# Optimization experiments

Measured on AMD Instinct MI355X. Metric: run time of the kernel, lower is better.

Reference implementation:

```python
import jax, jax.numpy as jnp
import numpy as np

N_NODES = 100000
N_EDGES = 3200000
IN_DIM, HID_DIM, OUT_DIM = 128, 8, 1


def _graph_conv(x, src, dst, W, b, n_nodes):
    """DGL GraphConv, norm='both', weight applied before aggregation
    (valid since in_feats > out_feats for both layers).
    out = D_in^{-1/2} * scatter_sum_dst( (D_out^{-1/2} * x W)[src] ) + b
    """
    ones_e = jnp.ones((src.shape[0],), dtype=x.dtype)
    deg_out = jax.ops.segment_sum(ones_e, src, num_segments=n_nodes)
    deg_in = jax.ops.segment_sum(ones_e, dst, num_segments=n_nodes)
    norm_out = jnp.clip(deg_out, 1.0, None) ** -0.5  # [N]
    norm_in = jnp.clip(deg_in, 1.0, None) ** -0.5    # [N]
    h = (x * norm_out[:, None]) @ W                   # [N, out_dim] small GEMM first
    msg = h[src]                                      # [E, out_dim] gather
    agg = jax.ops.segment_sum(msg, dst, num_segments=n_nodes)  # [N, out_dim] scatter
    return agg * norm_in[:, None] + b


def setup_inputs() -> dict:
    key = jax.random.key(0)
    k0, k1, k2, k3, k4, k5, k6 = jax.random.split(key, 7)
    x = jax.random.normal(k0, (N_NODES, IN_DIM), dtype=jnp.float32)
    src = jax.random.randint(k1, (N_EDGES,), 0, N_NODES, dtype=jnp.int64)
    dst = jax.random.randint(k2, (N_EDGES,), 0, N_NODES, dtype=jnp.int64)
    # Glorot-uniform weights as in DGL GraphConv reset_parameters
    lim1 = float(np.sqrt(6.0 / (IN_DIM + HID_DIM)))
    lim2 = float(np.sqrt(6.0 / (HID_DIM + OUT_DIM)))
    W1 = jax.random.uniform(k3, (IN_DIM, HID_DIM), minval=-lim1, maxval=lim1, dtype=jnp.float32)
    b1 = jnp.zeros((HID_DIM,), dtype=jnp.float32)
    W2 = jax.random.uniform(k4, (HID_DIM, OUT_DIM), minval=-lim2, maxval=lim2, dtype=jnp.float32)
    b2 = jnp.zeros((OUT_DIM,), dtype=jnp.float32)
    return {"x": x, "src": src, "dst": dst, "W1": W1, "b1": b1, "W2": W2, "b2": b2}


def reference(x, src, dst, W1, b1, W2, b2):
    h = _graph_conv(x, src, dst, W1, b1, N_NODES)   # conv1: 128 -> 8
    h = jax.nn.relu(h)
    out = _graph_conv(h, src, dst, W2, b2, N_NODES)  # conv2: 8 -> 1
    return out
```

## Files before the change

kernel.cpp:

```cpp
#include <hip/hip_runtime.h>
#include <hip/hip_bf16.h>
#include <hip/hip_fp16.h>

#define IN_DIM 128
#define HID 8
#define TW 256
#define MAXT 512
#define CCH 256
#define CAP 12288

__global__ __launch_bounds__(1024) void pass1AB_kernel(const int* __restrict__ src, const int* __restrict__ dst,
        int* __restrict__ cntS, int* __restrict__ cntD, int E, int RT, int chunk) {
    __shared__ int cs[MAXT], cd[MAXT];
    int t = threadIdx.x, c = blockIdx.x;
    for (int i = t; i < RT; i += 1024) { cs[i] = 0; cd[i] = 0; }
    __syncthreads();
    int lo = c * chunk, hi = min(lo + chunk, E);
    if (lo < hi) {
        const int4* s4 = reinterpret_cast<const int4*>(src);
        const int4* d4 = reinterpret_cast<const int4*>(dst);
        int q0 = lo >> 2, q1 = hi >> 2;
        for (int q = q0 + t; q < q1; q += 1024) {
            int4 s = s4[q], d = d4[q];
            atomicAdd(&cs[s.x >> 8], 1); atomicAdd(&cs[s.y >> 8], 1);
            atomicAdd(&cs[s.z >> 8], 1); atomicAdd(&cs[s.w >> 8], 1);
            atomicAdd(&cd[d.x >> 8], 1); atomicAdd(&cd[d.y >> 8], 1);
            atomicAdd(&cd[d.z >> 8], 1); atomicAdd(&cd[d.w >> 8], 1);
        }
        for (int i = (q1 << 2) + t; i < hi; i += 1024) {
            atomicAdd(&cs[src[i] >> 8], 1);
            atomicAdd(&cd[dst[i] >> 8], 1);
        }
    }
    __syncthreads();
    for (int i = t; i < RT; i += 1024) {
        cntS[(size_t)c * RT + i] = cs[i];
        cntD[(size_t)c * RT + i] = cd[i];
    }
}

__global__ __launch_bounds__(256) void scan1_kernel(int* __restrict__ cntS, int* __restrict__ cntD,
        int* __restrict__ totS, int* __restrict__ totD, int RT) {
    int r = blockIdx.x;
    int* cnt = blockIdx.y ? cntD : cntS;
    int* tot = blockIdx.y ? totD : totS;
    __shared__ int sh[256];
    int t = threadIdx.x;
    int e = cnt[(size_t)t * RT + r];
    sh[t] = e;
    __syncthreads();
    for (int off = 1; off < 256; off <<= 1) {
        int v = (t >= off) ? sh[t - off] : 0;
        __syncthreads();
        sh[t] += v;
        __syncthreads();
    }
    cnt[(size_t)t * RT + r] = sh[t] - e;
    if (t == 255) tot[r] = sh[255];
}

__global__ __launch_bounds__(256) void scan2_kernel(const int* __restrict__ totS, const int* __restrict__ totD,
        int* __restrict__ baseS, int* __restrict__ baseD, int RT) {
    const int* tot = blockIdx.x ? totD : totS;
    int* base = blockIdx.x ? baseD : baseS;
    __shared__ int sh[256];
    int t = threadIdx.x;
    int K = (RT + 255) / 256;
    int vals[4];
    int s = 0;
    for (int k = 0; k < K; ++k) {
        int i = t * K + k;
        int v = (i < RT) ? tot[i] : 0;
        vals[k] = v; s += v;
    }
    sh[t] = s;
    __syncthreads();
    for (int off = 1; off < 256; off <<= 1) {
        int v = (t >= off) ? sh[t - off] : 0;
        __syncthreads();
        sh[t] += v;
        __syncthreads();
    }
    int exc = sh[t] - s;
    for (int k = 0; k < K; ++k) {
        int i = t * K + k;
        if (i < RT) base[i] = exc;
        exc += vals[k];
    }
    if (t == 255) base[RT] = sh[255];
}

__global__ __launch_bounds__(1024) void scatterAB_kernel(const int* __restrict__ src, const int* __restrict__ dst,
        const int* __restrict__ cntS, const int* __restrict__ cntD,
        const int* __restrict__ baseS, const int* __restrict__ baseD,
        unsigned char* __restrict__ bucket_s, unsigned int* __restrict__ bucketT,
        int E, int RT, int chunk) {
    __shared__ int os[MAXT], od[MAXT];
    int t = threadIdx.x;
    int c = ((blockIdx.x & 7) << 5) | (blockIdx.x >> 3);
    for (int i = t; i < RT; i += 1024) {
        os[i] = baseS[i] + cntS[(size_t)c * RT + i];
        od[i] = baseD[i] + cntD[(size_t)c * RT + i];
    }
    __syncthreads();
    int lo = c * chunk, hi = min(lo + chunk, E);
    if (lo >= hi) return;
    const int4* s4 = reinterpret_cast<const int4*>(src);
    const int4* d4 = reinterpret_cast<const int4*>(dst);
    int q0 = lo >> 2, q1 = hi >> 2;
    for (int q = q0 + t; q < q1; q += 1024) {
        int4 s = s4[q], d = d4[q];
        int p;
        p = atomicAdd(&os[s.x >> 8], 1); bucket_s[p] = (unsigned char)(s.x & 255);
        p = atomicAdd(&os[s.y >> 8], 1); bucket_s[p] = (unsigned char)(s.y & 255);
        p = atomicAdd(&os[s.z >> 8], 1); bucket_s[p] = (unsigned char)(s.z & 255);
        p = atomicAdd(&os[s.w >> 8], 1); bucket_s[p] = (unsigned char)(s.w & 255);
        p = atomicAdd(&od[d.x >> 8], 1); bucketT[p] = ((unsigned)s.x << 8) | (unsigned)(d.x & 255);
        p = atomicAdd(&od[d.y >> 8], 1); bucketT[p] = ((unsigned)s.y << 8) | (unsigned)(d.y & 255);
        p = atomicAdd(&od[d.z >> 8], 1); bucketT[p] = ((unsigned)s.z << 8) | (unsigned)(d.z & 255);
        p = atomicAdd(&od[d.w >> 8], 1); bucketT[p] = ((unsigned)s.w << 8) | (unsigned)(d.w & 255);
    }
    for (int i = (q1 << 2) + t; i < hi; i += 1024) {
        int s = src[i], d = dst[i];
        int p = atomicAdd(&os[s >> 8], 1);
        bucket_s[p] = (unsigned char)(s & 255);
        p = atomicAdd(&od[d >> 8], 1);
        bucketT[p] = ((unsigned)s << 8) | (unsigned)(d & 255);
    }
}

__global__ __launch_bounds__(256) void conv1deg_kernel(
        const unsigned char* __restrict__ bucket_s, const int* __restrict__ baseS,
        const float* __restrict__ x, const float* __restrict__ W1,
        float* __restrict__ deg_out, uint4* __restrict__ h4, int N) {
    __shared__ float wt[HID * 132];
    __shared__ int cnt[TW];
    __shared__ float nrmS[TW];
    int r = blockIdx.x, t = threadIdx.x;
    for (int i = t; i < IN_DIM * HID; i += 256) {
        int k = i >> 3, j = i & 7;
        wt[j * 132 + k] = W1[i];
    }
    cnt[t] = 0;
    __syncthreads();
    int lo = baseS[r], hi = baseS[r + 1];
    int a0 = min((lo + 3) & ~3, hi), a1 = max(hi & ~3, a0);
    for (int i = lo + t; i < a0; i += 256) atomicAdd(&cnt[bucket_s[i]], 1);
    const unsigned* w4 = reinterpret_cast<const unsigned*>(bucket_s);
    for (int q = (a0 >> 2) + t; q < (a1 >> 2); q += 256) {
        unsigned w = w4[q];
        atomicAdd(&cnt[w & 255], 1);
        atomicAdd(&cnt[(w >> 8) & 255], 1);
        atomicAdd(&cnt[(w >> 16) & 255], 1);
        atomicAdd(&cnt[w >> 24], 1);
    }
    for (int i = a1 + t; i < hi; i += 256) atomicAdd(&cnt[bucket_s[i]], 1);
    __syncthreads();
    {
        int node = r * TW + t;
        if (node < N) deg_out[node] = (float)cnt[t];
        nrmS[t] = rsqrtf(fmaxf((float)cnt[t], 1.0f));
    }
    __syncthreads();
    int grp = t >> 3, lane = t & 7;
    #pragma unroll
    for (int sweep = 0; sweep < 8; ++sweep) {
        int nl = sweep * 32 + grp;
        int node = r * TW + nl;
        if (node < N) {
            const float4* xp = reinterpret_cast<const float4*>(x + (size_t)node * IN_DIM);
            float4 xv[4];
            #pragma unroll
            for (int m = 0; m < 4; ++m) xv[m] = xp[lane + m * 8];
            float acc[HID];
            #pragma unroll
            for (int j = 0; j < HID; ++j) acc[j] = 0.f;
            #pragma unroll
            for (int j = 0; j < HID; ++j) {
                #pragma unroll
                for (int m = 0; m < 4; ++m) {
                    float4 wv = *reinterpret_cast<const float4*>(&wt[j * 132 + lane * 4 + m * 32]);
                    acc[j] += xv[m].x * wv.x + xv[m].y * wv.y + xv[m].z * wv.z + xv[m].w * wv.w;
                }
            }
            #pragma unroll
            for (int off = 1; off < 8; off <<= 1) {
                #pragma unroll
                for (int j = 0; j < HID; ++j) acc[j] += __shfl_xor(acc[j], off, 64);
            }
            if (lane == 0) {
                float nrm = nrmS[nl];
                __half2 p0 = __floats2half2_rn(acc[0] * nrm, acc[1] * nrm);
                __half2 p1 = __floats2half2_rn(acc[2] * nrm, acc[3] * nrm);
                __half2 p2 = __floats2half2_rn(acc[4] * nrm, acc[5] * nrm);
                __half2 p3 = __floats2half2_rn(acc[6] * nrm, acc[7] * nrm);
                uint4 o;
                o.x = *reinterpret_cast<unsigned*>(&p0);
                o.y = *reinterpret_cast<unsigned*>(&p1);
                o.z = *reinterpret_cast<unsigned*>(&p2);
                o.w = *reinterpret_cast<unsigned*>(&p3);
                h4[node] = o;
            }
        }
    }
}

__device__ __forceinline__ void accAdd(float* acc, uint4 g) {
    __half2 q0 = *reinterpret_cast<__half2*>(&g.x);
    __half2 q1 = *reinterpret_cast<__half2*>(&g.y);
    __half2 q2 = *reinterpret_cast<__half2*>(&g.z);
    __half2 q3 = *reinterpret_cast<__half2*>(&g.w);
    float2 f0 = __half22float2(q0), f1 = __half22float2(q1);
    float2 f2 = __half22float2(q2), f3 = __half22float2(q3);
    acc[0] += f0.x; acc[1] += f0.y;
    acc[2] += f1.x; acc[3] += f1.y;
    acc[4] += f2.x; acc[5] += f2.y;
    acc[6] += f3.x; acc[7] += f3.y;
}

__global__ __launch_bounds__(512) void sortagg1_kernel(
        const unsigned int* __restrict__ bucketT, const int* __restrict__ baseD,
        unsigned int* __restrict__ bucketG, int* __restrict__ row_ptr,
        const uint4* __restrict__ h4, const float* __restrict__ deg_out,
        const float* __restrict__ b1, const float* __restrict__ W2,
        float* __restrict__ h2, int E, int RT, int N) {
    __shared__ unsigned sorted[CAP];
    __shared__ int cnt[TW], scn[TW], start[TW];
    __shared__ float b1s[HID], w2s[HID];
    int r = blockIdx.x, t = threadIdx.x;
    if (t < TW) cnt[t] = 0;
    if (t < HID) { b1s[t] = b1[t]; w2s[t] = W2[t]; }
    __syncthreads();
    int lo = baseD[r], hi = baseD[r + 1], len = hi - lo;
    for (int i = lo + t; i < hi; i += 512) atomicAdd(&cnt[bucketT[i] & 255u], 1);
    __syncthreads();
    if (t < TW) scn[t] = cnt[t];
    __syncthreads();
    for (int off = 1; off < TW; off <<= 1) {
        int v = 0;
        if (t < TW && t >= off) v = scn[t - off];
        __syncthreads();
        if (t < TW) scn[t] += v;
        __syncthreads();
    }
    if (t < TW) {
        start[t] = scn[t] - cnt[t];
        row_ptr[r * TW + t] = lo + scn[t] - cnt[t];
    }
    if (r == 0 && t == 0) row_ptr[RT * TW] = E;
    __syncthreads();
    bool fits = (len <= CAP);
    if (fits) {
        for (int i = lo + t; i < hi; i += 512) {
            unsigned v = bucketT[i];
            int p = atomicAdd(&start[v & 255u], 1);
            sorted[p] = v >> 8;
        }
        __syncthreads();
        for (int i = t; i < len; i += 512) bucketG[lo + i] = sorted[i];
    } else {
        for (int i = lo + t; i < hi; i += 512) {
            unsigned v = bucketT[i];
            int p = atomicAdd(&start[v & 255u], 1);
            bucketG[lo + p] = v >> 8;
        }
        __syncthreads();
    }
    #pragma unroll
    for (int half = 0; half < 2; ++half) {
        int nl = (t >> 2) + half * 128;
        int sub = t & 3;
        int node = r * TW + nl;
        int end = scn[nl], beg = end - cnt[nl];
        float acc[HID];
        #pragma unroll
        for (int j = 0; j < HID; ++j) acc[j] = 0.f;
        if (fits) {
            for (int e = beg + sub; e < end; e += 4) accAdd(acc, h4[sorted[e]]);
        } else {
            for (int e = beg + sub; e < end; e += 4) accAdd(acc, h4[bucketG[lo + e]]);
        }
        #pragma unroll
        for (int off = 1; off < 4; off <<= 1) {
            #pragma unroll
            for (int j = 0; j < HID; ++j) acc[j] += __shfl_xor(acc[j], off, 64);
        }
        if (sub == 0 && node < N) {
            float din = (float)(end - beg);
            float nin = rsqrtf(fmaxf(din, 1.f));
            float nout = rsqrtf(fmaxf(deg_out[node], 1.f));
            float dot = 0.f;
            #pragma unroll
            for (int j = 0; j < HID; ++j) {
                float y = fmaxf(acc[j] * nin + b1s[j], 0.f);
                dot += y * w2s[j];
            }
            h2[node] = dot * nout;
        }
    }
}

__global__ __launch_bounds__(256) void agg2G4_kernel(const unsigned int* __restrict__ bucketG,
        const int* __restrict__ row_ptr, const float* __restrict__ h2,
        const float* __restrict__ b2, float* __restrict__ out, int N) {
    int tid = blockIdx.x * 256 + threadIdx.x;
    int node = tid >> 2, sub = tid & 3;
    int s0 = row_ptr[node], s1 = row_ptr[node + 1];
    float a = 0.f;
    for (int e = s0 + sub; e < s1; e += 4) a += h2[bucketG[e]];
    a += __shfl_xor(a, 1, 64);
    a += __shfl_xor(a, 2, 64);
    if (sub == 0 && node < N) {
        float nin = rsqrtf(fmaxf((float)(s1 - s0), 1.f));
        out[node] = a * nin + b2[0];
    }
}

extern "C" void kernel_launch(void* const* d_in, const int* in_sizes, int n_in,
                              void* d_out, int out_size, void* d_ws, size_t ws_size,
                              hipStream_t stream) {
    const float* x  = (const float*)d_in[0];
    const int* src  = (const int*)d_in[1];
    const int* dst  = (const int*)d_in[2];
    const float* W1 = (const float*)d_in[3];
    const float* b1 = (const float*)d_in[4];
    const float* W2 = (const float*)d_in[5];
    const float* b2 = (const float*)d_in[6];
    float* out = (float*)d_out;

    const int N  = out_size;
    const int E  = in_sizes[1];
    const int RT = (N + TW - 1) / TW;
    const int chunk = (((E + CCH - 1) / CCH) + 3) & ~3;

    float* ws      = (float*)d_ws;
    float* deg_out = ws;
    float* h2      = deg_out + N;
    int*   cntS    = (int*)(h2 + N);
    int*   cntD    = cntS + (size_t)CCH * RT;
    int*   totS    = cntD + (size_t)CCH * RT;
    int*   baseS   = totS + RT;
    int*   totD    = baseS + RT + 1;
    int*   baseD   = totD + RT;
    int*   row_ptr = baseD + RT + 1;
    unsigned int* bucketT = (unsigned int*)(row_ptr + (size_t)RT * TW + 1);
    unsigned int* bucketG = bucketT + E;
    uint4* h4 = (uint4*)(((uintptr_t)(bucketG + E) + 15) & ~(uintptr_t)15);
    unsigned char* bucket_s = (unsigned char*)(h4 + N);

    pass1AB_kernel<<<CCH, 1024, 0, stream>>>(src, dst, cntS, cntD, E, RT, chunk);
    scan1_kernel<<<dim3(RT, 2), 256, 0, stream>>>(cntS, cntD, totS, totD, RT);
    scan2_kernel<<<2, 256, 0, stream>>>(totS, totD, baseS, baseD, RT);
    scatterAB_kernel<<<CCH, 1024, 0, stream>>>(src, dst, cntS, cntD, baseS, baseD,
                                               bucket_s, bucketT, E, RT, chunk);
    conv1deg_kernel<<<RT, 256, 0, stream>>>(bucket_s, baseS, x, W1, deg_out, h4, N);
    sortagg1_kernel<<<RT, 512, 0, stream>>>(bucketT, baseD, bucketG, row_ptr,
                                            h4, deg_out, b1, W2, h2, E, RT, N);
    agg2G4_kernel<<<RT * 4, 256, 0, stream>>>(bucketG, row_ptr, h2, b2, out, N);
}
```

Baseline: 113.9 us.

## Fuse conv1, sort-aggregate and layer-2 aggregation into one cooperative persistent kernel

Merges the three final kernels into a single cooperative kernel of 256 persistent blocks that loop over tiles and use grid-wide syncs between phases. Per-tile degree norms, row begins and counts stay in shared memory, which drops the deg_out and row_ptr global arrays. Tile width goes from 256 to 128 nodes, doubling the number of tiles and halving the sort buffer capacity. The aim is to cut launch gaps and global traffic. The cost is fewer resident blocks, serial tile loops per block, and more cases that fall back to the global-memory sort path.

```diff
diff --git a/kernel.cpp b/kernel.cpp
--- a/kernel.cpp
+++ b/kernel.cpp
@@ -1,13 +1,17 @@
 #include <hip/hip_runtime.h>
-#include <hip/hip_bf16.h>
+#include <hip/hip_cooperative_groups.h>
 #include <hip/hip_fp16.h>
+
+namespace cg = cooperative_groups;
 
 #define IN_DIM 128
 #define HID 8
-#define TW 256
-#define MAXT 512
+#define TW 128
+#define MAXT 1024
 #define CCH 256
-#define CAP 12288
+#define CAP 6144
+#define GRID 256
+#define KMAX 4
 
 __global__ __launch_bounds__(1024) void pass1AB_kernel(const int* __restrict__ src, const int* __restrict__ dst,
         int* __restrict__ cntS, int* __restrict__ cntD, int E, int RT, int chunk) {
@@ -22,14 +26,14 @@
         int q0 = lo >> 2, q1 = hi >> 2;
         for (int q = q0 + t; q < q1; q += 1024) {
             int4 s = s4[q], d = d4[q];
-            atomicAdd(&cs[s.x >> 8], 1); atomicAdd(&cs[s.y >> 8], 1);
-            atomicAdd(&cs[s.z >> 8], 1); atomicAdd(&cs[s.w >> 8], 1);
-            atomicAdd(&cd[d.x >> 8], 1); atomicAdd(&cd[d.y >> 8], 1);
-            atomicAdd(&cd[d.z >> 8], 1); atomicAdd(&cd[d.w >> 8], 1);
+            atomicAdd(&cs[s.x >> 7], 1); atomicAdd(&cs[s.y >> 7], 1);
+            atomicAdd(&cs[s.z >> 7], 1); atomicAdd(&cs[s.w >> 7], 1);
+            atomicAdd(&cd[d.x >> 7], 1); atomicAdd(&cd[d.y >> 7], 1);
+            atomicAdd(&cd[d.z >> 7], 1); atomicAdd(&cd[d.w >> 7], 1);
         }
         for (int i = (q1 << 2) + t; i < hi; i += 1024) {
-            atomicAdd(&cs[src[i] >> 8], 1);
-            atomicAdd(&cd[dst[i] >> 8], 1);
+            atomicAdd(&cs[src[i] >> 7], 1);
+            atomicAdd(&cd[dst[i] >> 7], 1);
         }
     }
     __syncthreads();
@@ -111,97 +115,21 @@
     for (int q = q0 + t; q < q1; q += 1024) {
         int4 s = s4[q], d = d4[q];
         int p;
-        p = atomicAdd(&os[s.x >> 8], 1); bucket_s[p] = (unsigned char)(s.x & 255);
-        p = atomicAdd(&os[s.y >> 8], 1); bucket_s[p] = (unsigned char)(s.y & 255);
-        p = atomicAdd(&os[s.z >> 8], 1); bucket_s[p] = (unsigned char)(s.z & 255);
-        p = atomicAdd(&os[s.w >> 8], 1); bucket_s[p] = (unsigned char)(s.w & 255);
-        p = atomicAdd(&od[d.x >> 8], 1); bucketT[p] = ((unsigned)s.x << 8) | (unsigned)(d.x & 255);
-        p = atomicAdd(&od[d.y >> 8], 1); bucketT[p] = ((unsigned)s.y << 8) | (unsigned)(d.y & 255);
-        p = atomicAdd(&od[d.z >> 8], 1); bucketT[p] = ((unsigned)s.z << 8) | (unsigned)(d.z & 255);
-        p = atomicAdd(&od[d.w >> 8], 1); bucketT[p] = ((unsigned)s.w << 8) | (unsigned)(d.w & 255);
+        p = atomicAdd(&os[s.x >> 7], 1); bucket_s[p] = (unsigned char)(s.x & 127);
+        p = atomicAdd(&os[s.y >> 7], 1); bucket_s[p] = (unsigned char)(s.y & 127);
+        p = atomicAdd(&os[s.z >> 7], 1); bucket_s[p] = (unsigned char)(s.z & 127);
+        p = atomicAdd(&os[s.w >> 7], 1); bucket_s[p] = (unsigned char)(s.w & 127);
+        p = atomicAdd(&od[d.x >> 7], 1); bucketT[p] = ((unsigned)s.x << 7) | (unsigned)(d.x & 127);
+        p = atomicAdd(&od[d.y >> 7], 1); bucketT[p] = ((unsigned)s.y << 7) | (unsigned)(d.y & 127);
+        p = atomicAdd(&od[d.z >> 7], 1); bucketT[p] = ((unsigned)s.z << 7) | (unsigned)(d.z & 127);
+        p = atomicAdd(&od[d.w >> 7], 1); bucketT[p] = ((unsigned)s.w << 7) | (unsigned)(d.w & 127);
     }
     for (int i = (q1 << 2) + t; i < hi; i += 1024) {
         int s = src[i], d = dst[i];
-        int p = atomicAdd(&os[s >> 8], 1);
-        bucket_s[p] = (unsigned char)(s & 255);
-        p = atomicAdd(&od[d >> 8], 1);
-        bucketT[p] = ((unsigned)s << 8) | (unsigned)(d & 255);
-    }
-}
-
-__global__ __launch_bounds__(256) void conv1deg_kernel(
-        const unsigned char* __restrict__ bucket_s, const int* __restrict__ baseS,
-        const float* __restrict__ x, const float* __restrict__ W1,
-        float* __restrict__ deg_out, uint4* __restrict__ h4, int N) {
-    __shared__ float wt[HID * 132];
-    __shared__ int cnt[TW];
-    __shared__ float nrmS[TW];
-    int r = blockIdx.x, t = threadIdx.x;
-    for (int i = t; i < IN_DIM * HID; i += 256) {
-        int k = i >> 3, j = i & 7;
-        wt[j * 132 + k] = W1[i];
-    }
-    cnt[t] = 0;
-    __syncthreads();
-    int lo = baseS[r], hi = baseS[r + 1];
-    int a0 = min((lo + 3) & ~3, hi), a1 = max(hi & ~3, a0);
-    for (int i = lo + t; i < a0; i += 256) atomicAdd(&cnt[bucket_s[i]], 1);
-    const unsigned* w4 = reinterpret_cast<const unsigned*>(bucket_s);
-    for (int q = (a0 >> 2) + t; q < (a1 >> 2); q += 256) {
-        unsigned w = w4[q];
-        atomicAdd(&cnt[w & 255], 1);
-        atomicAdd(&cnt[(w >> 8) & 255], 1);
-        atomicAdd(&cnt[(w >> 16) & 255], 1);
-        atomicAdd(&cnt[w >> 24], 1);
-    }
-    for (int i = a1 + t; i < hi; i += 256) atomicAdd(&cnt[bucket_s[i]], 1);
-    __syncthreads();
-    {
-        int node = r * TW + t;
-        if (node < N) deg_out[node] = (float)cnt[t];
-        nrmS[t] = rsqrtf(fmaxf((float)cnt[t], 1.0f));
-    }
-    __syncthreads();
-    int grp = t >> 3, lane = t & 7;
-    #pragma unroll
-    for (int sweep = 0; sweep < 8; ++sweep) {
-        int nl = sweep * 32 + grp;
-        int node = r * TW + nl;
-        if (node < N) {
-            const float4* xp = reinterpret_cast<const float4*>(x + (size_t)node * IN_DIM);
-            float4 xv[4];
-            #pragma unroll
-            for (int m = 0; m < 4; ++m) xv[m] = xp[lane + m * 8];
-            float acc[HID];
-            #pragma unroll
-            for (int j = 0; j < HID; ++j) acc[j] = 0.f;
-            #pragma unroll
-            for (int j = 0; j < HID; ++j) {
-                #pragma unroll
-                for (int m = 0; m < 4; ++m) {
-                    float4 wv = *reinterpret_cast<const float4*>(&wt[j * 132 + lane * 4 + m * 32]);
-                    acc[j] += xv[m].x * wv.x + xv[m].y * wv.y + xv[m].z * wv.z + xv[m].w * wv.w;
-                }
-            }
-            #pragma unroll
-            for (int off = 1; off < 8; off <<= 1) {
-                #pragma unroll
-                for (int j = 0; j < HID; ++j) acc[j] += __shfl_xor(acc[j], off, 64);
-            }
-            if (lane == 0) {
-                float nrm = nrmS[nl];
-                __half2 p0 = __floats2half2_rn(acc[0] * nrm, acc[1] * nrm);
-                __half2 p1 = __floats2half2_rn(acc[2] * nrm, acc[3] * nrm);
-                __half2 p2 = __floats2half2_rn(acc[4] * nrm, acc[5] * nrm);
-                __half2 p3 = __floats2half2_rn(acc[6] * nrm, acc[7] * nrm);
-                uint4 o;
-                o.x = *reinterpret_cast<unsigned*>(&p0);
-                o.y = *reinterpret_cast<unsigned*>(&p1);
-                o.z = *reinterpret_cast<unsigned*>(&p2);
-                o.w = *reinterpret_cast<unsigned*>(&p3);
-                h4[node] = o;
-            }
-        }
+        int p = atomicAdd(&os[s >> 7], 1);
+        bucket_s[p] = (unsigned char)(s & 127);
+        p = atomicAdd(&od[d >> 7], 1);
+        bucketT[p] = ((unsigned)s << 7) | (unsigned)(d & 127);
     }
 }
 
@@ -218,101 +146,184 @@
     acc[6] += f3.x; acc[7] += f3.y;
 }
 
-__global__ __launch_bounds__(512) void sortagg1_kernel(
+__global__ __launch_bounds__(512) void mega_kernel(
+        const unsigned char* __restrict__ bucket_s, const int* __restrict__ baseS,
         const unsigned int* __restrict__ bucketT, const int* __restrict__ baseD,
-        unsigned int* __restrict__ bucketG, int* __restrict__ row_ptr,
-        const uint4* __restrict__ h4, const float* __restrict__ deg_out,
-        const float* __restrict__ b1, const float* __restrict__ W2,
-        float* __restrict__ h2, int E, int RT, int N) {
+        const float* __restrict__ x, const float* __restrict__ W1,
+        const float* __restrict__ b1, const float* __restrict__ W2, const float* __restrict__ b2,
+        uint4* __restrict__ h4, unsigned int* __restrict__ bucketG,
+        float* __restrict__ h2, float* __restrict__ out, int RT, int N) {
+    __shared__ float wt[HID * 132];
     __shared__ unsigned sorted[CAP];
     __shared__ int cnt[TW], scn[TW], start[TW];
+    __shared__ float noutS[KMAX][TW];
+    __shared__ int begs[KMAX][TW], cnts[KMAX][TW];
     __shared__ float b1s[HID], w2s[HID];
-    int r = blockIdx.x, t = threadIdx.x;
-    if (t < TW) cnt[t] = 0;
+    __shared__ float b2s;
+    cg::grid_group gg = cg::this_grid();
+    int t = threadIdx.x, bid = blockIdx.x;
+    for (int i = t; i < IN_DIM * HID; i += 512) {
+        int k = i >> 3, j = i & 7;
+        wt[j * 132 + k] = W1[i];
+    }
     if (t < HID) { b1s[t] = b1[t]; w2s[t] = W2[t]; }
-    __syncthreads();
-    int lo = baseD[r], hi = baseD[r + 1], len = hi - lo;
-    for (int i = lo + t; i < hi; i += 512) atomicAdd(&cnt[bucketT[i] & 255u], 1);
-    __syncthreads();
-    if (t < TW) scn[t] = cnt[t];
-    __syncthreads();
-    for (int off = 1; off < TW; off <<= 1) {
-        int v = 0;
-        if (t < TW && t >= off) v = scn[t - off];
-        __syncthreads();
-        if (t < TW) scn[t] += v;
-        __syncthreads();
-    }
-    if (t < TW) {
-        start[t] = scn[t] - cnt[t];
-        row_ptr[r * TW + t] = lo + scn[t] - cnt[t];
-    }
-    if (r == 0 && t == 0) row_ptr[RT * TW] = E;
-    __syncthreads();
-    bool fits = (len <= CAP);
-    if (fits) {
-        for (int i = lo + t; i < hi; i += 512) {
-            unsigned v = bucketT[i];
-            int p = atomicAdd(&start[v & 255u], 1);
-            sorted[p] = v >> 8;
-        }
-        __syncthreads();
-        for (int i = t; i < len; i += 512) bucketG[lo + i] = sorted[i];
-    } else {
-        for (int i = lo + t; i < hi; i += 512) {
-            unsigned v = bucketT[i];
-            int p = atomicAdd(&start[v & 255u], 1);
-            bucketG[lo + p] = v >> 8;
-        }
-        __syncthreads();
-    }
-    #pragma unroll
-    for (int half = 0; half < 2; ++half) {
-        int nl = (t >> 2) + half * 128;
-        int sub = t & 3;
-        int node = r * TW + nl;
-        int end = scn[nl], beg = end - cnt[nl];
-        float acc[HID];
-        #pragma unroll
-        for (int j = 0; j < HID; ++j) acc[j] = 0.f;
-        if (fits) {
-            for (int e = beg + sub; e < end; e += 4) accAdd(acc, h4[sorted[e]]);
-        } else {
-            for (int e = beg + sub; e < end; e += 4) accAdd(acc, h4[bucketG[lo + e]]);
-        }
-        #pragma unroll
-        for (int off = 1; off < 4; off <<= 1) {
+    if (t == 0) b2s = b2[0];
+
+    {
+        int k = 0;
+        for (int r = bid; r < RT; r += GRID, ++k) {
+            __syncthreads();
+            if (t < TW) cnt[t] = 0;
+            __syncthreads();
+            int lo = baseS[r], hi = baseS[r + 1];
+            int a0 = min((lo + 3) & ~3, hi), a1 = max(hi & ~3, a0);
+            for (int i = lo + t; i < a0; i += 512) atomicAdd(&cnt[bucket_s[i]], 1);
+            const unsigned* w4 = reinterpret_cast<const unsigned*>(bucket_s);
+            for (int q = (a0 >> 2) + t; q < (a1 >> 2); q += 512) {
+                unsigned w = w4[q];
+                atomicAdd(&cnt[w & 255], 1);
+                atomicAdd(&cnt[(w >> 8) & 255], 1);
+                atomicAdd(&cnt[(w >> 16) & 255], 1);
+                atomicAdd(&cnt[w >> 24], 1);
+            }
+            for (int i = a1 + t; i < hi; i += 512) atomicAdd(&cnt[bucket_s[i]], 1);
+            __syncthreads();
+            if (t < TW) noutS[k][t] = rsqrtf(fmaxf((float)cnt[t], 1.0f));
+            __syncthreads();
+            int grp = t >> 3, lane = t & 7;
             #pragma unroll
-            for (int j = 0; j < HID; ++j) acc[j] += __shfl_xor(acc[j], off, 64);
-        }
-        if (sub == 0 && node < N) {
-            float din = (float)(end - beg);
-            float nin = rsqrtf(fmaxf(din, 1.f));
-            float nout = rsqrtf(fmaxf(deg_out[node], 1.f));
-            float dot = 0.f;
+            for (int sweep = 0; sweep < 2; ++sweep) {
+                int nl = sweep * 64 + grp;
+                int node = r * TW + nl;
+                if (node < N) {
+                    const float4* xp = reinterpret_cast<const float4*>(x + (size_t)node * IN_DIM);
+                    float4 xv[4];
+                    #pragma unroll
+                    for (int m = 0; m < 4; ++m) xv[m] = xp[lane + m * 8];
+                    float acc[HID];
+                    #pragma unroll
+                    for (int j = 0; j < HID; ++j) acc[j] = 0.f;
+                    #pragma unroll
+                    for (int j = 0; j < HID; ++j) {
+                        #pragma unroll
+                        for (int m = 0; m < 4; ++m) {
+                            float4 wv = *reinterpret_cast<const float4*>(&wt[j * 132 + lane * 4 + m * 32]);
+                            acc[j] += xv[m].x * wv.x + xv[m].y * wv.y + xv[m].z * wv.z + xv[m].w * wv.w;
+                        }
+                    }
+                    #pragma unroll
+                    for (int off = 1; off < 8; off <<= 1) {
+                        #pragma unroll
+                        for (int j = 0; j < HID; ++j) acc[j] += __shfl_xor(acc[j], off, 64);
+                    }
+                    if (lane == 0) {
+                        float nrm = noutS[k][nl];
+                        __half2 p0 = __floats2half2_rn(acc[0] * nrm, acc[1] * nrm);
+                        __half2 p1 = __floats2half2_rn(acc[2] * nrm, acc[3] * nrm);
+                        __half2 p2 = __floats2half2_rn(acc[4] * nrm, acc[5] * nrm);
+                        __half2 p3 = __floats2half2_rn(acc[6] * nrm, acc[7] * nrm);
+                        uint4 o;
+                        o.x = *reinterpret_cast<unsigned*>(&p0);
+                        o.y = *reinterpret_cast<unsigned*>(&p1);
+                        o.z = *reinterpret_cast<unsigned*>(&p2);
+                        o.w = *reinterpret_cast<unsigned*>(&p3);
+                        h4[node] = o;
+                    }
+                }
+            }
+        }
+    }
+    gg.sync();
+
+    {
+        int k = 0;
+        for (int r = bid; r < RT; r += GRID, ++k) {
+            __syncthreads();
+            if (t < TW) cnt[t] = 0;
+            __syncthreads();
+            int lo = baseD[r], hi = baseD[r + 1], len = hi - lo;
+            for (int i = lo + t; i < hi; i += 512) atomicAdd(&cnt[bucketT[i] & 127u], 1);
+            __syncthreads();
+            if (t < TW) scn[t] = cnt[t];
+            __syncthreads();
+            for (int off = 1; off < TW; off <<= 1) {
+                int v = 0;
+                if (t < TW && t >= off) v = scn[t - off];
+                __syncthreads();
+                if (t < TW) scn[t] += v;
+                __syncthreads();
+            }
+            if (t < TW) {
+                int b = scn[t] - cnt[t];
+                start[t] = b;
+                begs[k][t] = b;
+                cnts[k][t] = cnt[t];
+            }
+            __syncthreads();
+            bool fits = (len <= CAP);
+            if (fits) {
+                for (int i = lo + t; i < hi; i += 512) {
+                    unsigned v = bucketT[i];
+                    int p = atomicAdd(&start[v & 127u], 1);
+                    sorted[p] = v >> 7;
+                }
+                __syncthreads();
+                for (int i = t; i < len; i += 512) bucketG[lo + i] = sorted[i];
+            } else {
+                for (int i = lo + t; i < hi; i += 512) {
+                    unsigned v = bucketT[i];
+                    int p = atomicAdd(&start[v & 127u], 1);
+                    bucketG[lo + p] = v >> 7;
+                }
+                __syncthreads();
+            }
+            int nl = t >> 2, sub = t & 3;
+            int node = r * TW + nl;
+            int beg = begs[k][nl], end = beg + cnts[k][nl];
+            float acc[HID];
             #pragma unroll
-            for (int j = 0; j < HID; ++j) {
-                float y = fmaxf(acc[j] * nin + b1s[j], 0.f);
-                dot += y * w2s[j];
-            }
-            h2[node] = dot * nout;
-        }
-    }
-}
-
-__global__ __launch_bounds__(256) void agg2G4_kernel(const unsigned int* __restrict__ bucketG,
-        const int* __restrict__ row_ptr, const float* __restrict__ h2,
-        const float* __restrict__ b2, float* __restrict__ out, int N) {
-    int tid = blockIdx.x * 256 + threadIdx.x;
-    int node = tid >> 2, sub = tid & 3;
-    int s0 = row_ptr[node], s1 = row_ptr[node + 1];
-    float a = 0.f;
-    for (int e = s0 + sub; e < s1; e += 4) a += h2[bucketG[e]];
-    a += __shfl_xor(a, 1, 64);
-    a += __shfl_xor(a, 2, 64);
-    if (sub == 0 && node < N) {
-        float nin = rsqrtf(fmaxf((float)(s1 - s0), 1.f));
-        out[node] = a * nin + b2[0];
+            for (int j = 0; j < HID; ++j) acc[j] = 0.f;
+            if (fits) {
+                for (int e = beg + sub; e < end; e += 4) accAdd(acc, h4[sorted[e]]);
+            } else {
+                for (int e = beg + sub; e < end; e += 4) accAdd(acc, h4[bucketG[lo + e]]);
+            }
+            #pragma unroll
+            for (int off = 1; off < 4; off <<= 1) {
+                #pragma unroll
+                for (int j = 0; j < HID; ++j) acc[j] += __shfl_xor(acc[j], off, 64);
+            }
+            if (sub == 0 && node < N) {
+                float din = (float)(end - beg);
+                float nin = rsqrtf(fmaxf(din, 1.f));
+                float nout = noutS[k][nl];
+                float dot = 0.f;
+                #pragma unroll
+                for (int j = 0; j < HID; ++j) {
+                    float y = fmaxf(acc[j] * nin + b1s[j], 0.f);
+                    dot += y * w2s[j];
+                }
+                h2[node] = dot * nout;
+            }
+        }
+    }
+    gg.sync();
+
+    {
+        int k = 0;
+        for (int r = bid; r < RT; r += GRID, ++k) {
+            int lo = baseD[r];
+            int nl = t >> 2, sub = t & 3;
+            int node = r * TW + nl;
+            int beg = begs[k][nl], end = beg + cnts[k][nl];
+            float a = 0.f;
+            for (int e = beg + sub; e < end; e += 4) a += h2[bucketG[lo + e]];
+            a += __shfl_xor(a, 1, 64);
+            a += __shfl_xor(a, 2, 64);
+            if (sub == 0 && node < N) {
+                out[node] = a * rsqrtf(fmaxf((float)(end - beg), 1.f)) + b2s;
+            }
+        }
     }
 }
 
@@ -334,16 +345,14 @@
     const int chunk = (((E + CCH - 1) / CCH) + 3) & ~3;
 
     float* ws      = (float*)d_ws;
-    float* deg_out = ws;
-    float* h2      = deg_out + N;
+    float* h2      = ws;
     int*   cntS    = (int*)(h2 + N);
     int*   cntD    = cntS + (size_t)CCH * RT;
     int*   totS    = cntD + (size_t)CCH * RT;
     int*   baseS   = totS + RT;
     int*   totD    = baseS + RT + 1;
     int*   baseD   = totD + RT;
-    int*   row_ptr = baseD + RT + 1;
-    unsigned int* bucketT = (unsigned int*)(row_ptr + (size_t)RT * TW + 1);
+    unsigned int* bucketT = (unsigned int*)(baseD + RT + 1);
     unsigned int* bucketG = bucketT + E;
     uint4* h4 = (uint4*)(((uintptr_t)(bucketG + E) + 15) & ~(uintptr_t)15);
     unsigned char* bucket_s = (unsigned char*)(h4 + N);
@@ -353,8 +362,14 @@
     scan2_kernel<<<2, 256, 0, stream>>>(totS, totD, baseS, baseD, RT);
     scatterAB_kernel<<<CCH, 1024, 0, stream>>>(src, dst, cntS, cntD, baseS, baseD,
                                                bucket_s, bucketT, E, RT, chunk);
-    conv1deg_kernel<<<RT, 256, 0, stream>>>(bucket_s, baseS, x, W1, deg_out, h4, N);
-    sortagg1_kernel<<<RT, 512, 0, stream>>>(bucketT, baseD, bucketG, row_ptr,
-                                            h4, deg_out, b1, W2, h2, E, RT, N);
-    agg2G4_kernel<<<RT * 4, 256, 0, stream>>>(bucketG, row_ptr, h2, b2, out, N);
-}
+
+    int RT_arg = RT, N_arg = N;
+    void* args[] = {
+        (void*)&bucket_s, (void*)&baseS, (void*)&bucketT, (void*)&baseD,
+        (void*)&x, (void*)&W1, (void*)&b1, (void*)&W2, (void*)&b2,
+        (void*)&h4, (void*)&bucketG, (void*)&h2, (void*)&out,
+        (void*)&RT_arg, (void*)&N_arg
+    };
+    hipLaunchCooperativeKernel(reinterpret_cast<void*>(mega_kernel),
+                               dim3(GRID), dim3(512), args, 0, stream);
+}
```

New measurement: 204.8 us. 79.8% more time.
